# Performance work log

Measured on AMD Instinct MI355X. Metric: run time of the kernel, lower is better.

## Reference

```python
import jax, jax.numpy as jnp
import numpy as np

B, N2, N3 = 16, 618, 2466
FEAT, HID, EMB = 963, 192, 8
IN_DIM = FEAT + HID + EMB  # 1163
N_BLOCKS, DEG = 6, 6
N_NEW = N3 - N2  # 1848


def setup_inputs() -> dict:
    key = jax.random.key(0)
    ks = jax.random.split(key, 24)
    rng = np.random.default_rng(0)
    # sparse-structured row-normalized adjacency on the 2466-vertex mesh
    nbrs = rng.integers(0, N3, size=(N3, DEG))
    A = np.zeros((N3, N3), np.float32)
    A[np.arange(N3)[:, None], nbrs] = 1.0 / DEG
    unpool_idx = jnp.asarray(rng.integers(0, N2, size=(N_NEW, 2)), dtype=jnp.int32)
    s = 0.05
    d = {
        "x": jax.random.normal(ks[0], (B, N2, FEAT), jnp.float32),
        "x2": jax.random.normal(ks[1], (B, N2, 3), jnp.float32),
        "x_hidden": jax.random.normal(ks[2], (B, N2, HID), jnp.float32),
        # GA self-attention projections over 8-dim multivectors
        "Wq": jax.random.normal(ks[3], (EMB, EMB), jnp.float32) * s,
        "bq": jnp.zeros((EMB,), jnp.float32),
        "Wk": jax.random.normal(ks[4], (EMB, EMB), jnp.float32) * s,
        "bk": jnp.zeros((EMB,), jnp.float32),
        "Wv": jax.random.normal(ks[5], (EMB, EMB), jnp.float32) * s,
        "bv": jnp.zeros((EMB,), jnp.float32),
        "adj": jnp.asarray(A),
        "unpool_idx": unpool_idx,
        # GBottleneck: entry GConv
        "W_in": jax.random.normal(ks[6], (IN_DIM, HID), jnp.float32) * s,
        "loopW_in": jax.random.normal(ks[7], (IN_DIM, HID), jnp.float32) * s,
        "b_in": jnp.zeros((HID,), jnp.float32),
        # 6 GResBlocks x 2 GConvs each
        "res_W": jax.random.normal(ks[8], (N_BLOCKS, 2, HID, HID), jnp.float32) * s,
        "res_loopW": jax.random.normal(ks[9], (N_BLOCKS, 2, HID, HID), jnp.float32) * s,
        "res_b": jnp.zeros((N_BLOCKS, 2, HID), jnp.float32),
        # GBottleneck exit GConv (hidden -> last_hidden_dim)
        "W_out": jax.random.normal(ks[10], (HID, HID), jnp.float32) * s,
        "loopW_out": jax.random.normal(ks[11], (HID, HID), jnp.float32) * s,
        "b_out": jnp.zeros((HID,), jnp.float32),
        # final GConv to coordinates
        "Wg": jax.random.normal(ks[12], (HID, 3), jnp.float32) * s,
        "loopWg": jax.random.normal(ks[13], (HID, 3), jnp.float32) * s,
        "bg": jnp.zeros((3,), jnp.float32),
    }
    return d


def _gconv(h, adj, W, loopW, b):
    # GConv: adj @ (h W) + h W_loop + b
    return jnp.einsum("mn,bnf->bmf", adj, h @ W) + h @ loopW + b


def reference(x, x2, x_hidden, Wq, bq, Wk, bk, Wv, bv, adj, unpool_idx,
              W_in, loopW_in, b_in, res_W, res_loopW, res_b,
              W_out, loopW_out, b_out, Wg, loopWg, bg):
    # embed coords as grade-1 part of Cl(3,0) multivector: [B,N2,8]
    mv = jnp.zeros(x2.shape[:2] + (EMB,), x2.dtype).at[..., 1:4].set(x2)
    q = mv @ Wq + bq
    k = mv @ Wk + bk
    v = mv @ Wv + bv
    attn = jax.nn.softmax(jnp.einsum("bnd,bmd->bnm", q, k) / jnp.sqrt(jnp.float32(EMB)), axis=-1)
    x2_att = jnp.einsum("bnm,bmd->bnd", attn, v)  # [B,N2,8]
    feat = jnp.concatenate([x, x_hidden, x2_att], axis=2)  # [B,N2,1163]
    # GUnpooling: new vertices = midpoint of the two parents
    new_v = 0.5 * (feat[:, unpool_idx[:, 0]] + feat[:, unpool_idx[:, 1]])
    h = jnp.concatenate([feat, new_v], axis=1)  # [B,N3,1163]
    # GBottleneck: entry conv + 6 residual blocks
    h = jax.nn.relu(_gconv(h, adj, W_in, loopW_in, b_in))
    for i in range(N_BLOCKS):
        y = jax.nn.relu(_gconv(h, adj, res_W[i, 0], res_loopW[i, 0], res_b[i, 0]))
        y = jax.nn.relu(_gconv(y, adj, res_W[i, 1], res_loopW[i, 1], res_b[i, 1]))
        h = 0.5 * (h + y)
    x4 = _gconv(h, adj, W_out, loopW_out, b_out)  # GBottleneck output head
    x4 = jax.nn.relu(x4)  # gconv_activation=True
    x4 = _gconv(x4, adj, Wg, loopWg, bg)  # [B,N3,3]
    return x4
```

## Files before the change

kernel.cpp:

```cpp
#include <hip/hip_runtime.h>
#include <hip/hip_bf16.h>

#define NB 16
#define N2V 618
#define N3V 2466
#define FEAT 963
#define HID 192
#define IN_DIM 1163
#define KPAD2 1216
#define ETILES 38
#define EHALF 19
#define MTOT (NB * N3V)
#define M2   (NB * N2V)

typedef __attribute__((ext_vector_type(8))) short bf16x8;
typedef __attribute__((ext_vector_type(4))) float f32x4;

__device__ __forceinline__ float bf2f(ushort u) {
    return __uint_as_float(((unsigned)u) << 16);
}
__device__ __forceinline__ ushort f2bf(float f) {
    unsigned u = __float_as_uint(f);
    return (ushort)((u + 0x7FFFu + ((u >> 16) & 1u)) >> 16);
}
__device__ __forceinline__ int xcd_swz(int bid, int G) {
    int q = G >> 3, r = G & 7;
    int xcd = bid & 7, slot = bid >> 3;
    return (xcd < r) ? xcd * (q + 1) + slot : r * (q + 1) + (xcd - r) * q + slot;
}

__global__ void qkv_kernel(const float* __restrict__ x2,
                           const float* __restrict__ Wq, const float* __restrict__ bq,
                           const float* __restrict__ Wk, const float* __restrict__ bk,
                           const float* __restrict__ Wv, const float* __restrict__ bv,
                           float* __restrict__ q, float* __restrict__ k, float* __restrict__ v)
{
    int idx = blockIdx.x * 256 + threadIdx.x;
    if (idx >= M2) return;
    float c0 = x2[idx * 3 + 0], c1 = x2[idx * 3 + 1], c2 = x2[idx * 3 + 2];
#pragma unroll
    for (int d = 0; d < 8; ++d) {
        q[idx * 8 + d] = bq[d] + c0 * Wq[8 + d] + c1 * Wq[16 + d] + c2 * Wq[24 + d];
        k[idx * 8 + d] = bk[d] + c0 * Wk[8 + d] + c1 * Wk[16 + d] + c2 * Wk[24 + d];
        v[idx * 8 + d] = bv[d] + c0 * Wv[8 + d] + c1 * Wv[16 + d] + c2 * Wv[24 + d];
    }
}

__global__ __launch_bounds__(256) void attn_kernel2(const float* __restrict__ q,
                                                    const float* __restrict__ k,
                                                    const float* __restrict__ v,
                                                    float* __restrict__ att)
{
    __shared__ float4 kv[N2V * 4];
    int b = blockIdx.x, qb = blockIdx.y;
    const float4* k4 = (const float4*)(k + (size_t)b * N2V * 8);
    const float4* v4 = (const float4*)(v + (size_t)b * N2V * 8);
    for (int i = threadIdx.x; i < N2V * 2; i += 256) {
        kv[i] = k4[i];
        kv[N2V * 2 + i] = v4[i];
    }
    __syncthreads();

    int ql = threadIdx.x >> 2, sub = threadIdx.x & 3;
    int qi = qb * 64 + ql;
    bool valid = qi < N2V;
    float qv[8];
#pragma unroll
    for (int d = 0; d < 8; ++d) qv[d] = 0.f;
    if (valid) {
#pragma unroll
        for (int d = 0; d < 8; ++d) qv[d] = q[((size_t)b * N2V + qi) * 8 + d];
    }

    const float scale = 0.35355339059327373f;
    float m = -3.0e38f, lsum = 0.f, acc[8];
#pragma unroll
    for (int d = 0; d < 8; ++d) acc[d] = 0.f;

    for (int kk = sub; kk < N2V; kk += 4) {
        float4 k0 = kv[kk * 2], k1 = kv[kk * 2 + 1];
        float s = qv[0] * k0.x + qv[1] * k0.y + qv[2] * k0.z + qv[3] * k0.w
                + qv[4] * k1.x + qv[5] * k1.y + qv[6] * k1.z + qv[7] * k1.w;
        s *= scale;
        float nm = fmaxf(m, s);
        float corr = __expf(m - nm);
        float p = __expf(s - nm);
        lsum = lsum * corr + p;
        float4 v0 = kv[N2V * 2 + kk * 2], v1 = kv[N2V * 2 + kk * 2 + 1];
        acc[0] = acc[0] * corr + p * v0.x; acc[1] = acc[1] * corr + p * v0.y;
        acc[2] = acc[2] * corr + p * v0.z; acc[3] = acc[3] * corr + p * v0.w;
        acc[4] = acc[4] * corr + p * v1.x; acc[5] = acc[5] * corr + p * v1.y;
        acc[6] = acc[6] * corr + p * v1.z; acc[7] = acc[7] * corr + p * v1.w;
        m = nm;
    }
#pragma unroll
    for (int o = 1; o <= 2; o <<= 1) {
        float m2 = __shfl_xor(m, o);
        float l2 = __shfl_xor(lsum, o);
        float nm = fmaxf(m, m2);
        float c1 = __expf(m - nm), c2 = __expf(m2 - nm);
        lsum = lsum * c1 + l2 * c2;
#pragma unroll
        for (int d = 0; d < 8; ++d) {
            float a2 = __shfl_xor(acc[d], o);
            acc[d] = acc[d] * c1 + a2 * c2;
        }
        m = nm;
    }
    if (valid && sub == 0) {
#pragma unroll
        for (int d = 0; d < 8; ++d)
            att[((size_t)b * N2V + qi) * 8 + d] = acc[d] / lsum;
    }
}

__global__ void adj_prep(const float* __restrict__ adj, const int* __restrict__ unpool,
                         int* __restrict__ cols, float* __restrict__ vals,
                         int* __restrict__ eidx, float* __restrict__ ew,
                         int* __restrict__ sidx)
{
    int m = blockIdx.x;
    __shared__ int cnt;
    __shared__ int lc[8];
    __shared__ float lv[8];
    if (threadIdx.x == 0) cnt = 0;
    __syncthreads();
    for (int c = threadIdx.x; c < N3V; c += 256) {
        float a = adj[(size_t)m * N3V + c];
        if (a != 0.f) {
            int p = atomicAdd(&cnt, 1);
            if (p < 6) { lc[p] = c; lv[p] = a; }
        }
    }
    __syncthreads();
    if (threadIdx.x == 0) {
        int n = cnt < 6 ? cnt : 6;
        for (int i = 1; i < n; ++i) {
            int ci = lc[i]; float vi = lv[i]; int j = i - 1;
            while (j >= 0 && lc[j] > ci) { lc[j + 1] = lc[j]; lv[j + 1] = lv[j]; --j; }
            lc[j + 1] = ci; lv[j + 1] = vi;
        }
        int ne = 0;
        for (int i = 0; i < 6; ++i) {
            int c = (i < n) ? lc[i] : 0;
            float w = (i < n) ? lv[i] : 0.f;
            cols[m * 6 + i] = c;
            vals[m * 6 + i] = w;
            if (i < n) {
                if (c < N2V) { eidx[m * 12 + ne] = c; ew[m * 12 + ne] = w; ++ne; }
                else {
                    int jj = c - N2V;
                    eidx[m * 12 + ne] = unpool[2 * jj];     ew[m * 12 + ne] = 0.5f * w; ++ne;
                    eidx[m * 12 + ne] = unpool[2 * jj + 1]; ew[m * 12 + ne] = 0.5f * w; ++ne;
                }
            }
        }
        for (; ne < 12; ++ne) { eidx[m * 12 + ne] = 0; ew[m * 12 + ne] = 0.f; }
        if (m < N2V) { sidx[m * 2] = m; sidx[m * 2 + 1] = -1; }
        else {
            int j = m - N2V;
            sidx[m * 2] = unpool[2 * j];
            sidx[m * 2 + 1] = unpool[2 * j + 1];
        }
    }
}

__global__ void build_F3(const float* __restrict__ x, const float* __restrict__ xh,
                         const float* __restrict__ att, ushort* __restrict__ F3)
{
    int rt = blockIdx.x;
    for (int c = threadIdx.x; c < ETILES * 64; c += 256) {
        int kt = c >> 6, lane = c & 63;
        int row = rt * 16 + (lane & 15);
        int k0 = kt * 32 + (lane >> 4) * 8;
        bf16x8 o;
#pragma unroll
        for (int j = 0; j < 8; ++j) {
            int k = k0 + j;
            float v = 0.f;
            if (k < FEAT) v = x[(size_t)row * FEAT + k];
            else if (k < FEAT + HID) v = xh[(size_t)row * HID + (k - FEAT)];
            else if (k < IN_DIM) v = att[(size_t)row * 8 + (k - FEAT - HID)];
            o[j] = (short)f2bf(v);
        }
        *(bf16x8*)(F3 + ((size_t)(rt * ETILES + kt) * 64 + lane) * 8) = o;
    }
}

#define ENT_CHUNKS (24 * 38 * 64)
#define RES_CHUNKS (13 * 12 * 12 * 64)
__global__ void prep_wt_frag(const float* __restrict__ W_in, const float* __restrict__ loopW_in,
                             const float* __restrict__ res_W, const float* __restrict__ res_loopW,
                             const float* __restrict__ W_out, const float* __restrict__ loopW_out,
                             ushort* __restrict__ wt_e, ushort* __restrict__ wt_r)
{
    int idx = blockIdx.x * 256 + threadIdx.x;
    if (idx < ENT_CHUNKS) {
        int lane = idx & 63, r = idx >> 6;
        int kt = r % ETILES, ntile = r / ETILES;
        int n = ntile * 16 + (lane & 15);
        int k0 = kt * 32 + (lane >> 4) * 8;
        bf16x8 o;
#pragma unroll
        for (int j = 0; j < 8; ++j) {
            int k = k0 + j;
            float v = 0.f;
            if (k < IN_DIM) v = (n < 192) ? W_in[k * 192 + n] : loopW_in[k * 192 + (n - 192)];
            o[j] = (short)f2bf(v);
        }
        *(bf16x8*)(wt_e + (size_t)idx * 8) = o;
        return;
    }
    idx -= ENT_CHUNKS;
    if (idx >= RES_CHUNKS) return;
    int lane = idx & 63, r = idx >> 6;
    int kt = r % 12; r /= 12;
    int ntile = r % 12; int l = r / 12;
    const float* W = (l < 12) ? (res_W + (size_t)l * 192 * 192) : W_out;
    const float* L = (l < 12) ? (res_loopW + (size_t)l * 192 * 192) : loopW_out;
    int n = ntile * 16 + (lane & 15);
    int k0 = kt * 32 + (lane >> 4) * 8;
    bf16x8 o;
#pragma unroll
    for (int j = 0; j < 8; ++j) {
        int k2 = k0 + j;
        float v = (k2 < 192) ? W[k2 * 192 + n] : L[(k2 - 192) * 192 + n];
        o[j] = (short)f2bf(v);
    }
    *(bf16x8*)(wt_r + ((size_t)ENT_CHUNKS * 0) + ((size_t)(idx) * 8) + 0) = o;
}

__global__ __launch_bounds__(512) void gemm_entry(
    const ushort* __restrict__ F3, const ushort* __restrict__ Wt,
    ushort* __restrict__ u2)
{
    __shared__ float part[64 * 192];

    int tid = threadIdx.x;
    int wave = tid >> 6, lane = tid & 63;
    int kh = wave >> 2, w4 = wave & 3;
    int lr = lane & 15, lkq = lane >> 4;
    int row0 = blockIdx.x * 64;
    int rt0 = blockIdx.x * 4;
    int lnb = w4 * 48;
    int nb = blockIdx.y * 192 + lnb;
    int ntile0 = nb >> 4;
    int tbeg = kh * EHALF, tend = tbeg + EHALF;

    int rts[4];
#pragma unroll
    for (int mt = 0; mt < 4; ++mt) {
        int rt = rt0 + mt;
        rts[mt] = (rt < M2 / 16) ? rt : (M2 / 16 - 1);
    }

    f32x4 acc[4][3];
#pragma unroll
    for (int mt = 0; mt < 4; ++mt)
#pragma unroll
        for (int nt = 0; nt < 3; ++nt) acc[mt][nt] = (f32x4){0.f, 0.f, 0.f, 0.f};

    bf16x8 a0[4], b0[3], a1[4], b1[3];
    auto LD = [&](int t, bf16x8 (&a)[4], bf16x8 (&b)[3]) {
#pragma unroll
        for (int mt = 0; mt < 4; ++mt)
            a[mt] = *(const bf16x8*)(F3 + ((size_t)(rts[mt] * ETILES + t) * 64 + lane) * 8);
#pragma unroll
        for (int nt = 0; nt < 3; ++nt)
            b[nt] = *(const bf16x8*)(Wt + ((size_t)((ntile0 + nt) * ETILES + t) * 64 + lane) * 8);
    };
    auto MM = [&](bf16x8 (&a)[4], bf16x8 (&b)[3]) {
#pragma unroll
        for (int mt = 0; mt < 4; ++mt)
#pragma unroll
            for (int nt = 0; nt < 3; ++nt)
                acc[mt][nt] = __builtin_amdgcn_mfma_f32_16x16x32_bf16(a[mt], b[nt], acc[mt][nt], 0, 0, 0);
    };

    LD(tbeg, a0, b0);
    for (int t = tbeg; t < tend; t += 2) {
        if (t + 1 < tend) LD(t + 1, a1, b1);
        MM(a0, b0);
        if (t + 2 < tend) LD(t + 2, a0, b0);
        if (t + 1 < tend) MM(a1, b1);
    }

    int crow = lkq * 4;
    if (kh == 1) {
#pragma unroll
        for (int mt = 0; mt < 4; ++mt)
#pragma unroll
            for (int r = 0; r < 4; ++r)
#pragma unroll
                for (int nt = 0; nt < 3; ++nt)
                    part[(mt * 16 + crow + r) * 192 + lnb + nt * 16 + lr] = acc[mt][nt][r];
    }
    __syncthreads();
    if (kh == 0) {
#pragma unroll
        for (int mt = 0; mt < 4; ++mt)
#pragma unroll
            for (int r = 0; r < 4; ++r) {
                int orow = row0 + mt * 16 + crow + r;
                if (orow < M2) {
#pragma unroll
                    for (int nt = 0; nt < 3; ++nt) {
                        float s = acc[mt][nt][r] + part[(mt * 16 + crow + r) * 192 + lnb + nt * 16 + lr];
                        u2[(size_t)orow * 384 + nb + nt * 16 + lr] = f2bf(s);
                    }
                }
            }
    }
}

__global__ void combine_entry(const ushort* __restrict__ u2, const int* __restrict__ eidx,
                              const float* __restrict__ ew, const int* __restrict__ sidx,
                              const float* __restrict__ bias, ushort* __restrict__ h)
{
    int lb = xcd_swz(blockIdx.x, gridDim.x);
    int tid = threadIdx.x;
    int rloc = tid / 24, f8 = tid % 24;
    int bm = lb * 8 + rloc;
    if (bm >= MTOT) return;
    int b = bm / N3V, n = bm % N3V;
    const ushort* base = u2 + (size_t)b * N2V * 384;

    float acc[8];
#pragma unroll
    for (int e = 0; e < 8; ++e) acc[e] = 0.f;
#pragma unroll
    for (int i = 0; i < 12; ++i) {
        float w = ew[n * 12 + i];
        bf16x8 v = *(const bf16x8*)(base + (size_t)eidx[n * 12 + i] * 384 + f8 * 8);
#pragma unroll
        for (int e = 0; e < 8; ++e) acc[e] += w * bf2f((ushort)v[e]);
    }
    int p0 = sidx[n * 2], p1 = sidx[n * 2 + 1];
    bf16x8 s0 = *(const bf16x8*)(base + (size_t)p0 * 384 + 192 + f8 * 8);
    if (p1 >= 0) {
        bf16x8 s1 = *(const bf16x8*)(base + (size_t)p1 * 384 + 192 + f8 * 8);
#pragma unroll
        for (int e = 0; e < 8; ++e) acc[e] += 0.5f * (bf2f((ushort)s0[e]) + bf2f((ushort)s1[e]));
    } else {
#pragma unroll
        for (int e = 0; e < 8; ++e) acc[e] += bf2f((ushort)s0[e]);
    }
    bf16x8 o;
#pragma unroll
    for (int e = 0; e < 8; ++e)
        o[e] = (short)f2bf(fmaxf(acc[e] + bias[f8 * 8 + e], 0.f));
    *(bf16x8*)(h + (size_t)bm * 192 + f8 * 8) = o;
}

template <int ACT>
__global__ __launch_bounds__(512) void gconv_fused(
    const ushort* __restrict__ src, const int* __restrict__ cols,
    const float* __restrict__ vals, const ushort* __restrict__ Wt,
    const float* __restrict__ bias, const ushort* __restrict__ hprev,
    ushort* __restrict__ outp)
{
    __shared__ ushort gs[32 * 192];
    __shared__ float part[32 * 192];

    int lb = xcd_swz(blockIdx.x, gridDim.x);
    int tid = threadIdx.x;
    int row0 = lb * 32;

    for (int task = tid; task < 768; task += 512) {
        int r = task / 24, f8 = task % 24;
        int bm = row0 + r;
        int b = bm / N3V, m = bm % N3V;
        const ushort* hb = src + (size_t)b * N3V * 192;
        float acc[8];
#pragma unroll
        for (int e = 0; e < 8; ++e) acc[e] = 0.f;
#pragma unroll
        for (int j = 0; j < 6; ++j) {
            float w = vals[m * 6 + j];
            bf16x8 v = *(const bf16x8*)(hb + (size_t)cols[m * 6 + j] * 192 + f8 * 8);
#pragma unroll
            for (int e = 0; e < 8; ++e) acc[e] += w * bf2f((ushort)v[e]);
        }
        bf16x8 o;
#pragma unroll
        for (int e = 0; e < 8; ++e) o[e] = (short)f2bf(acc[e]);
        int byte = r * 384 + f8 * 16;
        byte ^= (r & 7) << 4;
        *(bf16x8*)((char*)gs + byte) = o;
    }
    __syncthreads();

    int wave = tid >> 6, lane = tid & 63;
    int kh = wave >> 2, w4 = wave & 3;
    int lr = lane & 15, lkq = lane >> 4, lk = lkq * 8;
    int nb = w4 * 48;
    int ntile0 = nb >> 4;
    int rows[2] = { row0 + lr, row0 + 16 + lr };
    int ktb = kh * 6;

    f32x4 acc[2][3];
#pragma unroll
    for (int mt = 0; mt < 2; ++mt)
#pragma unroll
        for (int nt = 0; nt < 3; ++nt) acc[mt][nt] = (f32x4){0.f, 0.f, 0.f, 0.f};

    bf16x8 a0[2], b0[3], a1[2], b1[3];
    auto LD = [&](int t, bf16x8 (&a)[2], bf16x8 (&b)[3]) {
        if (kh == 0) {
#pragma unroll
            for (int mt = 0; mt < 2; ++mt) {
                int rr = mt * 16 + lr;
                int byte = rr * 384 + t * 64 + lkq * 16;
                byte ^= (rr & 7) << 4;
                a[mt] = *(const bf16x8*)((const char*)gs + byte);
            }
        } else {
            int kk = t * 32 + lk;
#pragma unroll
            for (int mt = 0; mt < 2; ++mt)
                a[mt] = *(const bf16x8*)(src + (size_t)rows[mt] * 192 + kk);
        }
#pragma unroll
        for (int nt = 0; nt < 3; ++nt)
            b[nt] = *(const bf16x8*)(Wt + ((size_t)((ntile0 + nt) * 12 + ktb + t) * 64 + lane) * 8);
    };
    auto MM = [&](bf16x8 (&a)[2], bf16x8 (&b)[3]) {
#pragma unroll
        for (int mt = 0; mt < 2; ++mt)
#pragma unroll
            for (int nt = 0; nt < 3; ++nt)
                acc[mt][nt] = __builtin_amdgcn_mfma_f32_16x16x32_bf16(a[mt], b[nt], acc[mt][nt], 0, 0, 0);
    };

    LD(0, a0, b0);
#pragma unroll
    for (int t = 0; t < 6; t += 2) {
        if (t + 1 < 6) LD(t + 1, a1, b1);
        MM(a0, b0);
        if (t + 2 < 6) LD(t + 2, a0, b0);
        if (t + 1 < 6) MM(a1, b1);
    }

    int crow = lkq * 4;
    if (kh == 1) {
#pragma unroll
        for (int mt = 0; mt < 2; ++mt)
#pragma unroll
            for (int r = 0; r < 4; ++r)
#pragma unroll
                for (int nt = 0; nt < 3; ++nt)
                    part[(mt * 16 + crow + r) * 192 + nb + nt * 16 + lr] = acc[mt][nt][r];
    }
    __syncthreads();
    if (kh == 0) {
#pragma unroll
        for (int mt = 0; mt < 2; ++mt)
#pragma unroll
            for (int r = 0; r < 4; ++r) {
                int orow = row0 + mt * 16 + crow + r;
#pragma unroll
                for (int nt = 0; nt < 3; ++nt) {
                    int nn = nb + nt * 16 + lr;
                    float s = acc[mt][nt][r] + part[(mt * 16 + crow + r) * 192 + nn] + bias[nn];
                    s = fmaxf(s, 0.f);
                    if (ACT) s = 0.5f * (bf2f(hprev[(size_t)orow * 192 + nn]) + s);
                    outp[(size_t)orow * 192 + nn] = f2bf(s);
                }
            }
    }
}

__global__ void head_a2(const ushort* __restrict__ y, const float* __restrict__ Wg,
                        const float* __restrict__ loopWg, float* __restrict__ t)
{
    int tid = threadIdx.x;
    int rloc = tid >> 2, sub = tid & 3;
    int bm = blockIdx.x * 64 + rloc;
    if (bm >= MTOT) return;
    float s[6];
#pragma unroll
    for (int c = 0; c < 6; ++c) s[c] = 0.f;
#pragma unroll
    for (int kk = 0; kk < 6; ++kk) {
        int kg = sub * 6 + kk;
        bf16x8 v = *(const bf16x8*)(y + (size_t)bm * 192 + kg * 8);
#pragma unroll
        for (int e = 0; e < 8; ++e) {
            float f = bf2f((ushort)v[e]);
            int k = kg * 8 + e;
            s[0] += f * Wg[k * 3 + 0];
            s[1] += f * Wg[k * 3 + 1];
            s[2] += f * Wg[k * 3 + 2];
            s[3] += f * loopWg[k * 3 + 0];
            s[4] += f * loopWg[k * 3 + 1];
            s[5] += f * loopWg[k * 3 + 2];
        }
    }
#pragma unroll
    for (int o = 1; o <= 2; o <<= 1)
#pragma unroll
        for (int c = 0; c < 6; ++c) s[c] += __shfl_xor(s[c], o);
    if (sub == 0) {
#pragma unroll
        for (int c = 0; c < 6; ++c) t[(size_t)bm * 6 + c] = s[c];
    }
}

__global__ void head_b(const float* __restrict__ t, const int* __restrict__ cols,
                       const float* __restrict__ vals, const float* __restrict__ bg,
                       float* __restrict__ out)
{
    int idx = blockIdx.x * 256 + threadIdx.x;
    if (idx >= MTOT * 3) return;
    int bm = idx / 3, c = idx % 3;
    int b = bm / N3V, m = bm % N3V;
    float s = 0.f;
#pragma unroll
    for (int j = 0; j < 6; ++j)
        s += vals[m * 6 + j] * t[((size_t)b * N3V + cols[m * 6 + j]) * 6 + c];
    s += t[(size_t)bm * 6 + 3 + c] + bg[c];
    out[idx] = s;
}

extern "C" void kernel_launch(void* const* d_in, const int* in_sizes, int n_in,
                              void* d_out, int out_size, void* d_ws, size_t ws_size,
                              hipStream_t stream)
{
    const float* x        = (const float*)d_in[0];
    const float* x2       = (const float*)d_in[1];
    const float* xh       = (const float*)d_in[2];
    const float* Wq       = (const float*)d_in[3];
    const float* bq       = (const float*)d_in[4];
    const float* Wk       = (const float*)d_in[5];
    const float* bk       = (const float*)d_in[6];
    const float* Wv       = (const float*)d_in[7];
    const float* bv       = (const float*)d_in[8];
    const float* adj      = (const float*)d_in[9];
    const int*   unpool   = (const int*)d_in[10];
    const float* W_in     = (const float*)d_in[11];
    const float* loopW_in = (const float*)d_in[12];
    const float* b_in     = (const float*)d_in[13];
    const float* res_W    = (const float*)d_in[14];
    const float* res_loopW= (const float*)d_in[15];
    const float* res_b    = (const float*)d_in[16];
    const float* W_out    = (const float*)d_in[17];
    const float* loopW_out= (const float*)d_in[18];
    const float* b_out    = (const float*)d_in[19];
    const float* Wg       = (const float*)d_in[20];
    const float* loopWg   = (const float*)d_in[21];
    const float* bg       = (const float*)d_in[22];
    float* out = (float*)d_out;

    char* ws = (char*)d_ws;
    size_t o = 0;
    auto alloc = [&](size_t bytes) { char* p = ws + o; o += (bytes + 255) & ~(size_t)255; return p; };
    float*  q    = (float*)alloc((size_t)M2 * 8 * 4);
    float*  kbuf = (float*)alloc((size_t)M2 * 8 * 4);
    float*  vbuf = (float*)alloc((size_t)M2 * 8 * 4);
    float*  att  = (float*)alloc((size_t)M2 * 8 * 4);
    int*    cols = (int*)alloc((size_t)N3V * 6 * 4);
    float*  vals = (float*)alloc((size_t)N3V * 6 * 4);
    int*    eidx = (int*)alloc((size_t)N3V * 12 * 4);
    float*  ewgt = (float*)alloc((size_t)N3V * 12 * 4);
    int*    sidx = (int*)alloc((size_t)N3V * 2 * 4);
    ushort* F3   = (ushort*)alloc((size_t)M2 * KPAD2 * 2);
    ushort* wt_e = (ushort*)alloc((size_t)ENT_CHUNKS * 8 * 2);
    ushort* wt_r = (ushort*)alloc((size_t)RES_CHUNKS * 8 * 2);
    ushort* u2   = (ushort*)alloc((size_t)M2 * 384 * 2);
    ushort* h    = (ushort*)alloc((size_t)MTOT * 192 * 2);
    ushort* h2   = (ushort*)alloc((size_t)MTOT * 192 * 2);
    ushort* y    = (ushort*)alloc((size_t)MTOT * 192 * 2);
    float*  ts   = (float*)alloc((size_t)MTOT * 6 * 4);
    if (ws_size < o) return;

    qkv_kernel<<<(M2 + 255) / 256, 256, 0, stream>>>(x2, Wq, bq, Wk, bk, Wv, bv, q, kbuf, vbuf);
    attn_kernel2<<<dim3(NB, 10), 256, 0, stream>>>(q, kbuf, vbuf, att);
    adj_prep<<<N3V, 256, 0, stream>>>(adj, unpool, cols, vals, eidx, ewgt, sidx);
    build_F3<<<M2 / 16, 256, 0, stream>>>(x, xh, att, F3);
    prep_wt_frag<<<(ENT_CHUNKS + RES_CHUNKS + 255) / 256, 256, 0, stream>>>(
        W_in, loopW_in, res_W, res_loopW, W_out, loopW_out, wt_e, wt_r);

    gemm_entry<<<dim3((M2 + 63) / 64, 2), 512, 0, stream>>>(F3, wt_e, u2);
    combine_entry<<<(MTOT + 7) / 8, 192, 0, stream>>>(u2, eidx, ewgt, sidx, b_in, h);

    int gg = MTOT / 32;
    ushort* cur = h;
    ushort* nxt = h2;
    for (int i = 0; i < 6; ++i) {
        const float* B0 = res_b + (size_t)(i * 2 + 0) * 192;
        const float* B1 = res_b + (size_t)(i * 2 + 1) * 192;
        const ushort* W0 = wt_r + (size_t)(i * 2 + 0) * (12 * 12 * 64 * 8);
        const ushort* W1 = wt_r + (size_t)(i * 2 + 1) * (12 * 12 * 64 * 8);
        gconv_fused<0><<<gg, 512, 0, stream>>>(cur, cols, vals, W0, B0, nullptr, y);
        gconv_fused<1><<<gg, 512, 0, stream>>>(y, cols, vals, W1, B1, cur, nxt);
        ushort* tmp = cur; cur = nxt; nxt = tmp;
    }

    gconv_fused<0><<<gg, 512, 0, stream>>>(cur, cols, vals,
        wt_r + (size_t)12 * (12 * 12 * 64 * 8), b_out, nullptr, y);

    head_a2<<<(MTOT + 63) / 64, 256, 0, stream>>>(y, Wg, loopWg, ts);
    head_b<<<(MTOT * 3 + 255) / 256, 256, 0, stream>>>(ts, cols, vals, bg, out);
}
```

Measured before the change: 440.2 us.

## Overlap neighbor gather with self-loop MFMA and fuse QKV into attention

In the residual graph-conv kernel, the waves that previously did the self-loop half of the GEMM after a joint gather phase now run that GEMM concurrently while the other half of the waves perform the sparse neighbor gather into shared memory. The neighbor-half GEMM then runs after the barrier. This aims to hide gather latency behind tensor-core work instead of serializing them. Separately, the Q/K/V projection is folded into the attention kernel, removing one launch and the q/k/v round trip through global memory. The gather now uses only 256 threads for 768 tasks, so that phase may become longer and the overlap could be unbalanced.

```diff
diff --git a/kernel.cpp b/kernel.cpp
--- a/kernel.cpp
+++ b/kernel.cpp
@@ -29,35 +29,29 @@
     return (xcd < r) ? xcd * (q + 1) + slot : r * (q + 1) + (xcd - r) * q + slot;
 }
 
-__global__ void qkv_kernel(const float* __restrict__ x2,
-                           const float* __restrict__ Wq, const float* __restrict__ bq,
-                           const float* __restrict__ Wk, const float* __restrict__ bk,
-                           const float* __restrict__ Wv, const float* __restrict__ bv,
-                           float* __restrict__ q, float* __restrict__ k, float* __restrict__ v)
-{
-    int idx = blockIdx.x * 256 + threadIdx.x;
-    if (idx >= M2) return;
-    float c0 = x2[idx * 3 + 0], c1 = x2[idx * 3 + 1], c2 = x2[idx * 3 + 2];
-#pragma unroll
-    for (int d = 0; d < 8; ++d) {
-        q[idx * 8 + d] = bq[d] + c0 * Wq[8 + d] + c1 * Wq[16 + d] + c2 * Wq[24 + d];
-        k[idx * 8 + d] = bk[d] + c0 * Wk[8 + d] + c1 * Wk[16 + d] + c2 * Wk[24 + d];
-        v[idx * 8 + d] = bv[d] + c0 * Wv[8 + d] + c1 * Wv[16 + d] + c2 * Wv[24 + d];
-    }
-}
-
-__global__ __launch_bounds__(256) void attn_kernel2(const float* __restrict__ q,
-                                                    const float* __restrict__ k,
-                                                    const float* __restrict__ v,
-                                                    float* __restrict__ att)
+__global__ __launch_bounds__(256) void attn_fused(
+    const float* __restrict__ x2,
+    const float* __restrict__ Wq, const float* __restrict__ bq,
+    const float* __restrict__ Wk, const float* __restrict__ bk,
+    const float* __restrict__ Wv, const float* __restrict__ bv,
+    float* __restrict__ att)
 {
     __shared__ float4 kv[N2V * 4];
     int b = blockIdx.x, qb = blockIdx.y;
-    const float4* k4 = (const float4*)(k + (size_t)b * N2V * 8);
-    const float4* v4 = (const float4*)(v + (size_t)b * N2V * 8);
-    for (int i = threadIdx.x; i < N2V * 2; i += 256) {
-        kv[i] = k4[i];
-        kv[N2V * 2 + i] = v4[i];
+    const float* x2b = x2 + (size_t)b * N2V * 3;
+
+    for (int i = threadIdx.x; i < N2V; i += 256) {
+        float c0 = x2b[i * 3], c1 = x2b[i * 3 + 1], c2 = x2b[i * 3 + 2];
+        float kk[8], vv[8];
+#pragma unroll
+        for (int d = 0; d < 8; ++d) {
+            kk[d] = bk[d] + c0 * Wk[8 + d] + c1 * Wk[16 + d] + c2 * Wk[24 + d];
+            vv[d] = bv[d] + c0 * Wv[8 + d] + c1 * Wv[16 + d] + c2 * Wv[24 + d];
+        }
+        kv[i * 2]     = (float4){kk[0], kk[1], kk[2], kk[3]};
+        kv[i * 2 + 1] = (float4){kk[4], kk[5], kk[6], kk[7]};
+        kv[N2V * 2 + i * 2]     = (float4){vv[0], vv[1], vv[2], vv[3]};
+        kv[N2V * 2 + i * 2 + 1] = (float4){vv[4], vv[5], vv[6], vv[7]};
     }
     __syncthreads();
 
@@ -68,8 +62,10 @@
 #pragma unroll
     for (int d = 0; d < 8; ++d) qv[d] = 0.f;
     if (valid) {
-#pragma unroll
-        for (int d = 0; d < 8; ++d) qv[d] = q[((size_t)b * N2V + qi) * 8 + d];
+        float c0 = x2b[qi * 3], c1 = x2b[qi * 3 + 1], c2 = x2b[qi * 3 + 2];
+#pragma unroll
+        for (int d = 0; d < 8; ++d)
+            qv[d] = bq[d] + c0 * Wq[8 + d] + c1 * Wq[16 + d] + c2 * Wq[24 + d];
     }
 
     const float scale = 0.35355339059327373f;
@@ -227,7 +223,7 @@
         float v = (k2 < 192) ? W[k2 * 192 + n] : L[(k2 - 192) * 192 + n];
         o[j] = (short)f2bf(v);
     }
-    *(bf16x8*)(wt_r + ((size_t)ENT_CHUNKS * 0) + ((size_t)(idx) * 8) + 0) = o;
+    *(bf16x8*)(wt_r + (size_t)idx * 8) = o;
 }
 
 __global__ __launch_bounds__(512) void gemm_entry(
@@ -366,30 +362,6 @@
     int tid = threadIdx.x;
     int row0 = lb * 32;
 
-    for (int task = tid; task < 768; task += 512) {
-        int r = task / 24, f8 = task % 24;
-        int bm = row0 + r;
-        int b = bm / N3V, m = bm % N3V;
-        const ushort* hb = src + (size_t)b * N3V * 192;
-        float acc[8];
-#pragma unroll
-        for (int e = 0; e < 8; ++e) acc[e] = 0.f;
-#pragma unroll
-        for (int j = 0; j < 6; ++j) {
-            float w = vals[m * 6 + j];
-            bf16x8 v = *(const bf16x8*)(hb + (size_t)cols[m * 6 + j] * 192 + f8 * 8);
-#pragma unroll
-            for (int e = 0; e < 8; ++e) acc[e] += w * bf2f((ushort)v[e]);
-        }
-        bf16x8 o;
-#pragma unroll
-        for (int e = 0; e < 8; ++e) o[e] = (short)f2bf(acc[e]);
-        int byte = r * 384 + f8 * 16;
-        byte ^= (r & 7) << 4;
-        *(bf16x8*)((char*)gs + byte) = o;
-    }
-    __syncthreads();
-
     int wave = tid >> 6, lane = tid & 63;
     int kh = wave >> 2, w4 = wave & 3;
     int lr = lane & 15, lkq = lane >> 4, lk = lkq * 8;
@@ -405,20 +377,22 @@
         for (int nt = 0; nt < 3; ++nt) acc[mt][nt] = (f32x4){0.f, 0.f, 0.f, 0.f};
 
     bf16x8 a0[2], b0[3], a1[2], b1[3];
-    auto LD = [&](int t, bf16x8 (&a)[2], bf16x8 (&b)[3]) {
-        if (kh == 0) {
-#pragma unroll
-            for (int mt = 0; mt < 2; ++mt) {
-                int rr = mt * 16 + lr;
-                int byte = rr * 384 + t * 64 + lkq * 16;
-                byte ^= (rr & 7) << 4;
-                a[mt] = *(const bf16x8*)((const char*)gs + byte);
-            }
-        } else {
-            int kk = t * 32 + lk;
-#pragma unroll
-            for (int mt = 0; mt < 2; ++mt)
-                a[mt] = *(const bf16x8*)(src + (size_t)rows[mt] * 192 + kk);
+    auto LDself = [&](int t, bf16x8 (&a)[2], bf16x8 (&b)[3]) {
+        int kk = t * 32 + lk;
+#pragma unroll
+        for (int mt = 0; mt < 2; ++mt)
+            a[mt] = *(const bf16x8*)(src + (size_t)rows[mt] * 192 + kk);
+#pragma unroll
+        for (int nt = 0; nt < 3; ++nt)
+            b[nt] = *(const bf16x8*)(Wt + ((size_t)((ntile0 + nt) * 12 + ktb + t) * 64 + lane) * 8);
+    };
+    auto LDg = [&](int t, bf16x8 (&a)[2], bf16x8 (&b)[3]) {
+#pragma unroll
+        for (int mt = 0; mt < 2; ++mt) {
+            int rr = mt * 16 + lr;
+            int byte = rr * 384 + t * 64 + lkq * 16;
+            byte ^= (rr & 7) << 4;
+            a[mt] = *(const bf16x8*)((const char*)gs + byte);
         }
 #pragma unroll
         for (int nt = 0; nt < 3; ++nt)
@@ -432,17 +406,17 @@
                 acc[mt][nt] = __builtin_amdgcn_mfma_f32_16x16x32_bf16(a[mt], b[nt], acc[mt][nt], 0, 0, 0);
     };
 
-    LD(0, a0, b0);
-#pragma unroll
-    for (int t = 0; t < 6; t += 2) {
-        if (t + 1 < 6) LD(t + 1, a1, b1);
-        MM(a0, b0);
-        if (t + 2 < 6) LD(t + 2, a0, b0);
-        if (t + 1 < 6) MM(a1, b1);
-    }
-
     int crow = lkq * 4;
+
     if (kh == 1) {
+        LDself(0, a0, b0);
+#pragma unroll
+        for (int t = 0; t < 6; t += 2) {
+            if (t + 1 < 6) LDself(t + 1, a1, b1);
+            MM(a0, b0);
+            if (t + 2 < 6) LDself(t + 2, a0, b0);
+            if (t + 1 < 6) MM(a1, b1);
+        }
 #pragma unroll
         for (int mt = 0; mt < 2; ++mt)
 #pragma unroll
@@ -450,9 +424,43 @@
 #pragma unroll
                 for (int nt = 0; nt < 3; ++nt)
                     part[(mt * 16 + crow + r) * 192 + nb + nt * 16 + lr] = acc[mt][nt][r];
+    } else {
+#pragma unroll
+        for (int it = 0; it < 3; ++it) {
+            int task = tid + it * 256;
+            int r = task / 24, f8 = task % 24;
+            int bm = row0 + r;
+            int b = bm / N3V, m = bm % N3V;
+            const ushort* hb = src + (size_t)b * N3V * 192;
+            float ga[8];
+#pragma unroll
+            for (int e = 0; e < 8; ++e) ga[e] = 0.f;
+#pragma unroll
+            for (int j = 0; j < 6; ++j) {
+                float w = vals[m * 6 + j];
+                bf16x8 v = *(const bf16x8*)(hb + (size_t)cols[m * 6 + j] * 192 + f8 * 8);
+#pragma unroll
+                for (int e = 0; e < 8; ++e) ga[e] += w * bf2f((ushort)v[e]);
+            }
+            bf16x8 o;
+#pragma unroll
+            for (int e = 0; e < 8; ++e) o[e] = (short)f2bf(ga[e]);
+            int byte = r * 384 + f8 * 16;
+            byte ^= (r & 7) << 4;
+            *(bf16x8*)((char*)gs + byte) = o;
+        }
     }
     __syncthreads();
+
     if (kh == 0) {
+        LDg(0, a0, b0);
+#pragma unroll
+        for (int t = 0; t < 6; t += 2) {
+            if (t + 1 < 6) LDg(t + 1, a1, b1);
+            MM(a0, b0);
+            if (t + 2 < 6) LDg(t + 2, a0, b0);
+            if (t + 1 < 6) MM(a1, b1);
+        }
 #pragma unroll
         for (int mt = 0; mt < 2; ++mt)
 #pragma unroll
@@ -554,9 +562,6 @@
     char* ws = (char*)d_ws;
     size_t o = 0;
     auto alloc = [&](size_t bytes) { char* p = ws + o; o += (bytes + 255) & ~(size_t)255; return p; };
-    float*  q    = (float*)alloc((size_t)M2 * 8 * 4);
-    float*  kbuf = (float*)alloc((size_t)M2 * 8 * 4);
-    float*  vbuf = (float*)alloc((size_t)M2 * 8 * 4);
     float*  att  = (float*)alloc((size_t)M2 * 8 * 4);
     int*    cols = (int*)alloc((size_t)N3V * 6 * 4);
     float*  vals = (float*)alloc((size_t)N3V * 6 * 4);
@@ -573,8 +578,7 @@
     float*  ts   = (float*)alloc((size_t)MTOT * 6 * 4);
     if (ws_size < o) return;
 
-    qkv_kernel<<<(M2 + 255) / 256, 256, 0, stream>>>(x2, Wq, bq, Wk, bk, Wv, bv, q, kbuf, vbuf);
-    attn_kernel2<<<dim3(NB, 10), 256, 0, stream>>>(q, kbuf, vbuf, att);
+    attn_fused<<<dim3(NB, 10), 256, 0, stream>>>(x2, Wq, bq, Wk, bk, Wv, bv, att);
     adj_prep<<<N3V, 256, 0, stream>>>(adj, unpool, cols, vals, eidx, ewgt, sidx);
     build_F3<<<M2 / 16, 256, 0, stream>>>(x, xh, att, F3);
     prep_wt_frag<<<(ENT_CHUNKS + RES_CHUNKS + 255) / 256, 256, 0, stream>>>(
```

New measurement: 426.0 us. -3.2%, faster.
